# Kernel optimization log

Hardware: AMD Instinct MI355X
Metric: run time of the kernel (lower is better)

Reference implementation:

```python
import jax, jax.numpy as jnp
import numpy as np

N, E, D_IN, D_OUT = 100000, 1600000, 128, 128


def setup_inputs() -> dict:
    key = jax.random.key(0)
    k1, k2, k3, k4 = jax.random.split(key, 4)
    x = jax.random.normal(k1, (N, D_IN), dtype=jnp.float32)
    edge_index = jax.random.randint(k2, (2, E), 0, N, dtype=jnp.int64)
    # nn.Linear(in_feats, out_feats): W is (out, in) in torch; store (in, out) for x @ W
    bound = 1.0 / np.sqrt(D_IN)
    W = jax.random.uniform(k3, (D_IN, D_OUT), dtype=jnp.float32, minval=-bound, maxval=bound)
    b = jax.random.uniform(k4, (D_OUT,), dtype=jnp.float32, minval=-bound, maxval=bound)
    return {"x": x, "edge_index": edge_index, "W": W, "b": b}


def reference(x, edge_index, W, b):
    src, dst = edge_index[0], edge_index[1]
    # gather src features then scatter-sum into dst slots (dim_size=N)
    agg = jax.ops.segment_sum(x[src], dst, num_segments=N)  # (N, D_in)
    return agg @ W + b  # (N, D_out)
```

## Files before the change

### kernel.cpp

```cpp
#include <hip/hip_runtime.h>
#include <hip/hip_bf16.h>

#define D 128
#define GRP 64
#define NBMAX 4096
#define CAPB_MAX 2048

typedef __attribute__((ext_vector_type(8))) short short8;
typedef __attribute__((ext_vector_type(4))) float f32x4;

__device__ __forceinline__ float bf2f(unsigned short u) {
    union { unsigned int i; float f; } c;
    c.i = ((unsigned int)u) << 16;
    return c.f;
}
__device__ __forceinline__ float bits2f(unsigned int i) {
    union { unsigned int i; float f; } c;
    c.i = i;
    return c.f;
}
__device__ __forceinline__ unsigned short f2bf(float f) {
    __hip_bfloat16 h = __float2bfloat16(f);
    return *(unsigned short*)&h;
}

__device__ __forceinline__ int block_probe_xf32(const unsigned short* x) {
    __shared__ int cntS;
    if (threadIdx.x == 0) cntS = 0;
    __syncthreads();
    int bad = 0;
    for (int i = threadIdx.x; i < 512; i += blockDim.x) {
        float v = bf2f(x[i]);
        if (!(fabsf(v) < 1e4f)) bad++;
    }
    if (bad) atomicAdd(&cntS, bad);
    __syncthreads();
    int r = (cntS > 2) ? 1 : 0;
    __syncthreads();
    return r;
}
__device__ __forceinline__ int block_probe_i64(const void* eiv, int nNodes) {
    __shared__ int okS;
    if (threadIdx.x == 0) okS = 1;
    __syncthreads();
    if (threadIdx.x < 64) {
        long long v = ((const long long*)eiv)[threadIdx.x];
        if (v < 0 || v >= (long long)nNodes) atomicAnd(&okS, 0);
    }
    __syncthreads();
    int r = okS;
    __syncthreads();
    return r;
}

__global__ __launch_bounds__(64) void probe_kernel(
    const unsigned short* __restrict__ x,
    const long long* __restrict__ ei64,
    int nNodes, int* __restrict__ flags)
{
    const int lane = threadIdx.x;
    int cnt = 0;
    for (int i = lane; i < 512; i += 64) {
        float v = bf2f(x[i]);
        if (!(fabsf(v) < 1e4f)) cnt++;
    }
    unsigned long long m1 = __ballot(cnt > 0);
    long long v = ei64[lane];
    int bad = (v < 0 || v >= (long long)nNodes) ? 1 : 0;
    unsigned long long m2 = __ballot(bad);
    if (lane == 0) {
        flags[0] = (__popcll(m1) > 2) ? 1 : 0;
        flags[1] = (m2 == 0) ? 1 : 0;
    }
}

__global__ __launch_bounds__(256, 2) void gemm_mfma(
    const void* __restrict__ xv, const void* __restrict__ Wv, void* __restrict__ yv,
    int nNodes, int nTiles,
    int* __restrict__ zbase, int zInts, int* __restrict__ mhead, int NB)
{
    __shared__ unsigned short Wth[D * D];
    __shared__ unsigned short Wtl[D * D];

    const int tid = threadIdx.x;

    for (int i = blockIdx.x * 256 + tid; i < zInts; i += gridDim.x * 256) zbase[i] = 0;
    for (int i = blockIdx.x * 256 + tid; i < NB; i += gridDim.x * 256) mhead[i] = -1;

    const int xf32 = block_probe_xf32((const unsigned short*)xv);
    const int w = tid >> 6, l = tid & 63;
    const int lr = l & 15, g = l >> 4;

    if (xf32) {
        const float* W = (const float*)Wv;
        for (int i = tid; i < D * D; i += 256) {
            int c = i & 127, k = i >> 7;
            float wv = W[(size_t)k * D + c];
            unsigned short hi = f2bf(wv);
            unsigned short lo = f2bf(wv - bf2f(hi));
            int ba = (((c << 7) + k) << 1) ^ ((c & 7) << 4);
            *(unsigned short*)((char*)Wth + ba) = hi;
            *(unsigned short*)((char*)Wtl + ba) = lo;
        }
    } else {
        const unsigned short* W = (const unsigned short*)Wv;
        for (int i = tid; i < D * D / 2; i += 256) {
            int c = i & 127, k2 = i >> 7;
            unsigned int v0 = W[(size_t)(2 * k2) * D + c];
            unsigned int v1 = W[(size_t)(2 * k2 + 1) * D + c];
            unsigned int pk = v0 | (v1 << 16);
            int ba = (((c << 7) + 2 * k2) << 1) ^ ((c & 7) << 4);
            *(unsigned int*)((char*)Wth + ba) = pk;
        }
    }
    __syncthreads();

    unsigned short* y = (unsigned short*)yv;

    for (int t = blockIdx.x; t < nTiles; t += gridDim.x) {
        const int row0 = t * 64 + w * 16;
        int arow = row0 + lr; if (arow >= nNodes) arow = nNodes - 1;

        short8 ah[4], al[4];
        if (xf32) {
            const float* xr = (const float*)xv + (size_t)arow * D;
            #pragma unroll
            for (int kk = 0; kk < 4; ++kk) {
                float f[8];
                *(float4*)&f[0] = *(const float4*)(xr + kk * 32 + g * 8);
                *(float4*)&f[4] = *(const float4*)(xr + kk * 32 + g * 8 + 4);
                #pragma unroll
                for (int i = 0; i < 8; ++i) {
                    unsigned short hi = f2bf(f[i]);
                    ah[kk][i] = (short)hi;
                    al[kk][i] = (short)f2bf(f[i] - bf2f(hi));
                }
            }
        } else {
            const char* xrow = (const char*)xv + (size_t)arow * (D * 2);
            #pragma unroll
            for (int kk = 0; kk < 4; ++kk)
                ah[kk] = *(const short8*)(xrow + (kk << 6) + (g << 4));
        }

        #pragma unroll
        for (int c = 0; c < 8; ++c) {
            const int col = c * 16 + lr;
            f32x4 acc = {0.f, 0.f, 0.f, 0.f};
            #pragma unroll
            for (int kk = 0; kk < 4; ++kk) {
                int ba = ((col << 8) + (kk << 6) + (g << 4)) ^ ((col & 7) << 4);
                short8 bh = *(const short8*)((const char*)Wth + ba);
                acc = __builtin_amdgcn_mfma_f32_16x16x32_bf16(ah[kk], bh, acc, 0, 0, 0);
                if (xf32) {
                    short8 bl = *(const short8*)((const char*)Wtl + ba);
                    acc = __builtin_amdgcn_mfma_f32_16x16x32_bf16(ah[kk], bl, acc, 0, 0, 0);
                    acc = __builtin_amdgcn_mfma_f32_16x16x32_bf16(al[kk], bh, acc, 0, 0, 0);
                }
            }
            #pragma unroll
            for (int j = 0; j < 4; ++j) {
                int row = row0 + g * 4 + j;
                if (row < nNodes)
                    y[(size_t)row * D + col] = f2bf(acc[j]);
            }
        }
    }
}

__global__ __launch_bounds__(256) void gemm_kernel(
    const void* __restrict__ inv, const void* __restrict__ Wv,
    const void* __restrict__ bv, void* __restrict__ outv,
    int nNodes, const int* __restrict__ flags,
    int in_f32p, int out_f32p, int add_bias)
{
    __shared__ float Ws[D * D];
    __shared__ float bs[D];

    const int xf32 = flags[0];
    const int in_f32  = (in_f32p  < 0) ? xf32 : in_f32p;
    const int out_f32 = (out_f32p < 0) ? xf32 : out_f32p;

    if (xf32) {
        const float* W = (const float*)Wv;
        for (int i = threadIdx.x; i < D * D; i += 256) Ws[i] = W[i];
        if (threadIdx.x < D)
            bs[threadIdx.x] = add_bias ? ((const float*)bv)[threadIdx.x] : 0.f;
    } else {
        const unsigned short* W = (const unsigned short*)Wv;
        for (int i = threadIdx.x; i < D * D; i += 256) Ws[i] = bf2f(W[i]);
        if (threadIdx.x < D)
            bs[threadIdx.x] = add_bias ? bf2f(((const unsigned short*)bv)[threadIdx.x]) : 0.f;
    }
    __syncthreads();

    const int cg = threadIdx.x & 31;
    const int rg = threadIdx.x >> 5;
    const int c = cg * 4;
    const int row0 = blockIdx.x * 64 + rg * 8;

    size_t rIdx[8];
    #pragma unroll
    for (int r = 0; r < 8; ++r) {
        int row = row0 + r;
        rIdx[r] = (size_t)(row < nNodes ? row : nNodes - 1);
    }

    float4 acc[8];
    #pragma unroll
    for (int r = 0; r < 8; ++r)
        acc[r] = make_float4(bs[c], bs[c + 1], bs[c + 2], bs[c + 3]);

    if (in_f32) {
        const float* in = (const float*)inv;
        for (int k = 0; k < D; k += 4) {
            float4 w0 = *(const float4*)&Ws[(k + 0) * D + c];
            float4 w1 = *(const float4*)&Ws[(k + 1) * D + c];
            float4 w2 = *(const float4*)&Ws[(k + 2) * D + c];
            float4 w3 = *(const float4*)&Ws[(k + 3) * D + c];
            #pragma unroll
            for (int r = 0; r < 8; ++r) {
                float4 a = *(const float4*)(in + rIdx[r] * D + k);
                acc[r].x += a.x * w0.x + a.y * w1.x + a.z * w2.x + a.w * w3.x;
                acc[r].y += a.x * w0.y + a.y * w1.y + a.z * w2.y + a.w * w3.y;
                acc[r].z += a.x * w0.z + a.y * w1.z + a.z * w2.z + a.w * w3.z;
                acc[r].w += a.x * w0.w + a.y * w1.w + a.z * w2.w + a.w * w3.w;
            }
        }
    } else {
        const unsigned short* in = (const unsigned short*)inv;
        for (int k = 0; k < D; k += 4) {
            float4 w0 = *(const float4*)&Ws[(k + 0) * D + c];
            float4 w1 = *(const float4*)&Ws[(k + 1) * D + c];
            float4 w2 = *(const float4*)&Ws[(k + 2) * D + c];
            float4 w3 = *(const float4*)&Ws[(k + 3) * D + c];
            #pragma unroll
            for (int r = 0; r < 8; ++r) {
                ushort4 u = *(const ushort4*)(in + rIdx[r] * D + k);
                float ax = bf2f(u.x), ay = bf2f(u.y), az = bf2f(u.z), aw = bf2f(u.w);
                acc[r].x += ax * w0.x + ay * w1.x + az * w2.x + aw * w3.x;
                acc[r].y += ax * w0.y + ay * w1.y + az * w2.y + aw * w3.y;
                acc[r].z += ax * w0.z + ay * w1.z + az * w2.z + aw * w3.z;
                acc[r].w += ax * w0.w + ay * w1.w + az * w2.w + aw * w3.w;
            }
        }
    }

    #pragma unroll
    for (int r = 0; r < 8; ++r) {
        int row = row0 + r;
        if (row >= nNodes) break;
        if (out_f32) {
            ((float4*)outv)[(size_t)row * 32 + cg] = acc[r];
        } else {
            ushort4 o;
            o.x = f2bf(acc[r].x); o.y = f2bf(acc[r].y);
            o.z = f2bf(acc[r].z); o.w = f2bf(acc[r].w);
            ((ushort4*)outv)[(size_t)row * 32 + cg] = o;
        }
    }
}

__global__ __launch_bounds__(256) void bin_edges(
    const void* __restrict__ eiv, int* __restrict__ gcnt, unsigned int* __restrict__ grp,
    int* __restrict__ ovfCnt, int* __restrict__ ovfHead, int2* __restrict__ ovf,
    int nEdges, int nNodes, int NB, int CAPB, int nPer)
{
    __shared__ int cnts[NBMAX];
    __shared__ int run[NBMAX];

    const int i64 = block_probe_i64(eiv, nNodes);

    const int e0 = blockIdx.x * nPer;
    int e1 = e0 + nPer; if (e1 > nEdges) e1 = nEdges;
    const long long* ei64 = (const long long*)eiv;
    const int* ei32 = (const int*)eiv;

    for (int i = threadIdx.x; i < NB; i += 256) cnts[i] = 0;
    __syncthreads();

    for (int e = e0 + threadIdx.x; e < e1; e += 256) {
        int d = i64 ? (int)ei64[(size_t)nEdges + e] : ei32[(size_t)nEdges + e];
        atomicAdd(&cnts[d >> 6], 1);
    }
    __syncthreads();

    for (int g = threadIdx.x; g < NB; g += 256) {
        int c = cnts[g];
        run[g] = (c > 0) ? atomicAdd(&gcnt[(size_t)g * 16], c) : 0;
    }
    __syncthreads();

    for (int e = e0 + threadIdx.x; e < e1; e += 256) {
        int s, d;
        if (i64) { s = (int)ei64[e]; d = (int)ei64[(size_t)nEdges + e]; }
        else     { s = ei32[e];      d = ei32[(size_t)nEdges + e]; }
        int g = d >> 6;
        int pos = atomicAdd(&run[g], 1);
        unsigned int p = (unsigned int)s | ((unsigned int)(d & 63) << 20);
        if (pos < CAPB) {
            grp[(size_t)g * CAPB + pos] = p;
        } else {
            int idx = atomicAdd(ovfCnt, 1);
            int old = atomicExch(&ovfHead[g], idx);
            ovf[idx] = make_int2(old, (int)p);
        }
    }
}

__global__ __launch_bounds__(256, 4) void sort_accum(
    const void* __restrict__ xv,
    const unsigned int* __restrict__ yu,
    const int* __restrict__ gcnt, const unsigned int* __restrict__ grp,
    const int* __restrict__ ovfHead, const int2* __restrict__ ovf,
    const void* __restrict__ bv, void* __restrict__ outv,
    int nNodes, int CAPB)
{
    __shared__ unsigned int sorted[CAPB_MAX];
    __shared__ int rcnt[GRP], roff[GRP], rrun[GRP];

    const int xf32 = block_probe_xf32((const unsigned short*)xv);

    const int g = blockIdx.x;
    const int n0 = g << 6;
    const int tid = threadIdx.x;
    const int w = tid >> 6, lane = tid & 63;

    if (tid < GRP) rcnt[tid] = 0;
    __syncthreads();

    const int cnt = gcnt[(size_t)g * 16];
    const int m = cnt < CAPB ? cnt : CAPB;

    for (int i = tid; i < m; i += 256)
        atomicAdd(&rcnt[grp[(size_t)g * CAPB + i] >> 20], 1);
    __syncthreads();

    if (w == 0) {
        int v = rcnt[lane];
        int sc = v;
        #pragma unroll
        for (int o = 1; o < 64; o <<= 1) {
            int t = __shfl_up(sc, o);
            if (lane >= o) sc += t;
        }
        roff[lane] = sc - v;
        rrun[lane] = sc - v;
    }
    __syncthreads();

    for (int i = tid; i < m; i += 256) {
        unsigned int p = grp[(size_t)g * CAPB + i];
        int pos = atomicAdd(&rrun[p >> 20], 1);
        sorted[pos] = p & 0xFFFFFu;
    }
    __syncthreads();

    const bool hasOvf = (cnt > CAPB);

    for (int r = w; r < GRP; r += 4) {
        int node = n0 + r;
        if (node >= nNodes) break;
        const int j0 = roff[r], dg = rcnt[r];

        float a0 = 0.f, a1 = 0.f, a2 = 0.f, a3 = 0.f;
        float b0 = 0.f, b1 = 0.f, b2 = 0.f, b3 = 0.f;
        int j = 0;
        for (; j + 4 <= dg; j += 4) {
            unsigned int s0 = sorted[j0 + j + 0];
            unsigned int s1 = sorted[j0 + j + 1];
            unsigned int s2 = sorted[j0 + j + 2];
            unsigned int s3 = sorted[j0 + j + 3];
            unsigned int u0 = yu[(size_t)s0 * 64 + lane];
            unsigned int u1 = yu[(size_t)s1 * 64 + lane];
            unsigned int u2 = yu[(size_t)s2 * 64 + lane];
            unsigned int u3 = yu[(size_t)s3 * 64 + lane];
            a0 += bits2f(u0 << 16); b0 += bits2f(u0 & 0xFFFF0000u);
            a1 += bits2f(u1 << 16); b1 += bits2f(u1 & 0xFFFF0000u);
            a2 += bits2f(u2 << 16); b2 += bits2f(u2 & 0xFFFF0000u);
            a3 += bits2f(u3 << 16); b3 += bits2f(u3 & 0xFFFF0000u);
        }
        for (; j < dg; ++j) {
            unsigned int s0 = sorted[j0 + j];
            unsigned int u0 = yu[(size_t)s0 * 64 + lane];
            a0 += bits2f(u0 << 16); b0 += bits2f(u0 & 0xFFFF0000u);
        }

        if (hasOvf) {
            int cur = ovfHead[g];
            while (cur >= 0) {
                int2 t = ovf[cur];
                unsigned int p = (unsigned int)t.y;
                if ((int)(p >> 20) == r) {
                    unsigned int u = yu[(size_t)(p & 0xFFFFFu) * 64 + lane];
                    a0 += bits2f(u << 16); b0 += bits2f(u & 0xFFFF0000u);
                }
                cur = t.x;
            }
        }

        float f0 = (a0 + a1) + (a2 + a3);
        float f1 = (b0 + b1) + (b2 + b3);

        if (xf32) {
            float2 bb = ((const float2*)bv)[lane];
            float2 o; o.x = f0 + bb.x; o.y = f1 + bb.y;
            ((float2*)outv)[(size_t)node * 64 + lane] = o;
        } else {
            unsigned int ub = ((const unsigned int*)bv)[lane];
            f0 += bits2f(ub << 16);
            f1 += bits2f(ub & 0xFFFF0000u);
            unsigned int o = ((unsigned int)f2bf(f0)) | (((unsigned int)f2bf(f1)) << 16);
            ((unsigned int*)outv)[(size_t)node * 64 + lane] = o;
        }
    }
}

__global__ __launch_bounds__(256) void scatter_kernel(
    const void* __restrict__ xv, const void* __restrict__ eiv,
    float* __restrict__ agg, int nEdges, const int* __restrict__ flags)
{
    long long tid = (long long)blockIdx.x * 256 + threadIdx.x;
    int e = (int)(tid >> 5);
    if (e >= nEdges) return;
    int q = (int)tid & 31;

    const int xf32 = flags[0];
    int s, d;
    if (flags[1]) {
        const long long* ei = (const long long*)eiv;
        s = (int)ei[e]; d = (int)ei[(size_t)nEdges + e];
    } else {
        const int* ei = (const int*)eiv;
        s = ei[e]; d = ei[(size_t)nEdges + e];
    }
    float4 v;
    if (xf32) {
        v = ((const float4*)xv)[(size_t)s * 32 + q];
    } else {
        ushort4 u = ((const ushort4*)xv)[(size_t)s * 32 + q];
        v.x = bf2f(u.x); v.y = bf2f(u.y); v.z = bf2f(u.z); v.w = bf2f(u.w);
    }
    float* ap = agg + (size_t)d * D + q * 4;
    atomicAdd(ap + 0, v.x);
    atomicAdd(ap + 1, v.y);
    atomicAdd(ap + 2, v.z);
    atomicAdd(ap + 3, v.w);
}

static inline size_t alignup(size_t v, size_t a) { return (v + a - 1) & ~(a - 1); }

extern "C" void kernel_launch(void* const* d_in, const int* in_sizes, int n_in,
                              void* d_out, int out_size, void* d_ws, size_t ws_size,
                              hipStream_t stream) {
    const void* x  = d_in[0];
    const void* ei = d_in[1];
    const void* W  = d_in[2];
    const void* b  = d_in[3];

    const int nNodes = in_sizes[0] / D;
    const int nEdges = in_sizes[1] / 2;
    const int NB = (nNodes + GRP - 1) / GRP;

    int CAPB = 0;
    size_t off_gcnt = 512, off_ovfc = 0, off_head = 0, off_ovf = 0, off_grp = 0, off_y = 0;
    if (nNodes < (1 << 20) && NB <= NBMAX) {
        int cap = CAPB_MAX;
        size_t ogcnt = 512;
        size_t oovfc = alignup(ogcnt + 64ull * NB, 256);
        size_t ohead = oovfc + 256;
        size_t oovf  = alignup(ohead + 4ull * NB, 256);
        size_t ogrp  = alignup(oovf + 8ull * nEdges, 256);
        size_t oy    = alignup(ogrp + 4ull * cap * NB, 512);
        size_t need  = oy + (size_t)nNodes * D * 2;
        if (ws_size >= need) {
            CAPB = cap; off_gcnt = ogcnt; off_ovfc = oovfc; off_head = ohead;
            off_ovf = oovf; off_grp = ogrp; off_y = oy;
        }
    }

    const int mblocks = (nNodes + 63) / 64;

    if (CAPB > 0) {
        int*          gcnt    = (int*)((char*)d_ws + off_gcnt);
        int*          ovfCnt  = (int*)((char*)d_ws + off_ovfc);
        int*          ovfHead = (int*)((char*)d_ws + off_head);
        int2*         ovf     = (int2*)((char*)d_ws + off_ovf);
        unsigned int* grp     = (unsigned int*)((char*)d_ws + off_grp);
        void*         y       = (void*)((char*)d_ws + off_y);

        const int zInts = (int)((off_head - off_gcnt) / 4);

        int gblocks = mblocks < 512 ? mblocks : 512;
        gemm_mfma<<<gblocks, 256, 0, stream>>>(x, W, y, nNodes, mblocks,
                                               gcnt, zInts, ovfHead, NB);

        const int ABLK = 1024;
        const int nPer = (nEdges + ABLK - 1) / ABLK;
        bin_edges<<<ABLK, 256, 0, stream>>>(ei, gcnt, grp, ovfCnt, ovfHead, ovf,
                                            nEdges, nNodes, NB, CAPB, nPer);

        sort_accum<<<NB, 256, 0, stream>>>(x, (const unsigned int*)y, gcnt, grp,
                                           ovfHead, ovf, b, d_out,
                                           nNodes, CAPB);
    } else {
        int* flags = (int*)d_ws;
        probe_kernel<<<1, 64, 0, stream>>>((const unsigned short*)x, (const long long*)ei,
                                           nNodes, flags);
        float* agg = (float*)((char*)d_ws + 512);
        hipMemsetAsync(agg, 0, (size_t)nNodes * D * sizeof(float), stream);
        long long total = (long long)nEdges * 32;
        int sblocks = (int)((total + 255) / 256);
        scatter_kernel<<<sblocks, 256, 0, stream>>>(x, ei, agg, nEdges, flags);
        gemm_kernel<<<mblocks, 256, 0, stream>>>(agg, W, b, d_out, nNodes, flags,
                                                 1, -1, 1);
    }
}
```

Baseline: 274.2 us.

## Stage binned edges in LDS via local prefix sum before writing to global bins

```diff
diff --git a/kernel.cpp b/kernel.cpp
--- a/kernel.cpp
+++ b/kernel.cpp
@@ -5,6 +5,7 @@
 #define GRP 64
 #define NBMAX 4096
 #define CAPB_MAX 2048
+#define STAGE_E 8192
 
 typedef __attribute__((ext_vector_type(8))) short short8;
 typedef __attribute__((ext_vector_type(4))) float f32x4;
@@ -267,44 +268,84 @@
     int nEdges, int nNodes, int NB, int CAPB, int nPer)
 {
     __shared__ int cnts[NBMAX];
-    __shared__ int run[NBMAX];
+    __shared__ int lrun[NBMAX];
+    __shared__ int gbase[NBMAX];
+    __shared__ unsigned int stage[STAGE_E];
+    __shared__ int wsum[4];
 
     const int i64 = block_probe_i64(eiv, nNodes);
-
-    const int e0 = blockIdx.x * nPer;
-    int e1 = e0 + nPer; if (e1 > nEdges) e1 = nEdges;
+    const int tid = threadIdx.x;
+    const int lane = tid & 63, wv = tid >> 6;
     const long long* ei64 = (const long long*)eiv;
     const int* ei32 = (const int*)eiv;
 
-    for (int i = threadIdx.x; i < NB; i += 256) cnts[i] = 0;
-    __syncthreads();
-
-    for (int e = e0 + threadIdx.x; e < e1; e += 256) {
-        int d = i64 ? (int)ei64[(size_t)nEdges + e] : ei32[(size_t)nEdges + e];
-        atomicAdd(&cnts[d >> 6], 1);
-    }
-    __syncthreads();
-
-    for (int g = threadIdx.x; g < NB; g += 256) {
-        int c = cnts[g];
-        run[g] = (c > 0) ? atomicAdd(&gcnt[(size_t)g * 16], c) : 0;
-    }
-    __syncthreads();
-
-    for (int e = e0 + threadIdx.x; e < e1; e += 256) {
-        int s, d;
-        if (i64) { s = (int)ei64[e]; d = (int)ei64[(size_t)nEdges + e]; }
-        else     { s = ei32[e];      d = ei32[(size_t)nEdges + e]; }
-        int g = d >> 6;
-        int pos = atomicAdd(&run[g], 1);
-        unsigned int p = (unsigned int)s | ((unsigned int)(d & 63) << 20);
-        if (pos < CAPB) {
-            grp[(size_t)g * CAPB + pos] = p;
-        } else {
-            int idx = atomicAdd(ovfCnt, 1);
-            int old = atomicExch(&ovfHead[g], idx);
-            ovf[idx] = make_int2(old, (int)p);
-        }
+    const int e0 = blockIdx.x * nPer;
+    int eEnd = e0 + nPer; if (eEnd > nEdges) eEnd = nEdges;
+
+    for (int ch = e0; ch < eEnd; ch += STAGE_E) {
+        int ce = ch + STAGE_E; if (ce > eEnd) ce = eEnd;
+
+        for (int i = tid; i < NB; i += 256) cnts[i] = 0;
+        __syncthreads();
+
+        for (int e = ch + tid; e < ce; e += 256) {
+            int d = i64 ? (int)ei64[(size_t)nEdges + e] : ei32[(size_t)nEdges + e];
+            atomicAdd(&cnts[d >> 6], 1);
+        }
+        __syncthreads();
+
+        const int chunk = (NB + 255) / 256;
+        const int g0 = tid * chunk;
+        int g1 = g0 + chunk; if (g1 > NB) g1 = NB;
+        int run = 0;
+        for (int g = g0; g < g1; ++g) {
+            lrun[g] = run;
+            run += cnts[g];
+            gbase[g] = (cnts[g] > 0) ? atomicAdd(&gcnt[(size_t)g * 16], cnts[g]) : 0;
+        }
+        int sc = run;
+        #pragma unroll
+        for (int o = 1; o < 64; o <<= 1) {
+            int t = __shfl_up(sc, o);
+            if (lane >= o) sc += t;
+        }
+        if (lane == 63) wsum[wv] = sc;
+        __syncthreads();
+        int wbase = 0;
+        for (int i = 0; i < wv; ++i) wbase += wsum[i];
+        const int tbase = wbase + sc - run;
+        for (int g = g0; g < g1; ++g) lrun[g] += tbase;
+        __syncthreads();
+
+        for (int e = ch + tid; e < ce; e += 256) {
+            int s, d;
+            if (i64) { s = (int)ei64[e]; d = (int)ei64[(size_t)nEdges + e]; }
+            else     { s = ei32[e];      d = ei32[(size_t)nEdges + e]; }
+            int g = d >> 6;
+            unsigned int p = (unsigned int)s | ((unsigned int)(d & 63) << 20);
+            int pos = atomicAdd(&lrun[g], 1);
+            stage[pos] = p;
+        }
+        __syncthreads();
+
+        for (int g = tid; g < NB; g += 256) {
+            int c = cnts[g];
+            if (c == 0) continue;
+            int st = lrun[g] - c;
+            int gb = gbase[g];
+            for (int i = 0; i < c; ++i) {
+                unsigned int p = stage[st + i];
+                int pos = gb + i;
+                if (pos < CAPB) {
+                    grp[(size_t)g * CAPB + pos] = p;
+                } else {
+                    int idx = atomicAdd(ovfCnt, 1);
+                    int old = atomicExch(&ovfHead[g], idx);
+                    ovf[idx] = make_int2(old, (int)p);
+                }
+            }
+        }
+        __syncthreads();
     }
 }
 
@@ -495,7 +536,7 @@
         gemm_mfma<<<gblocks, 256, 0, stream>>>(x, W, y, nNodes, mblocks,
                                                gcnt, zInts, ovfHead, NB);
 
-        const int ABLK = 1024;
+        const int ABLK = 256;
         const int nPer = (nEdges + ABLK - 1) / ABLK;
         bin_edges<<<ABLK, 256, 0, stream>>>(ei, gcnt, grp, ovfCnt, ovfHead, ovf,
                                             nEdges, nNodes, NB, CAPB, nPer);
```

Result: faster. 239.7 us, median of 2 (-12.6%).
